# Optimization experiments

Hardware: AMD Instinct MI355X
Metric: run time of the kernel (lower is better)

Reference implementation:

```python
import jax, jax.numpy as jnp
import numpy as np

NEG_INF = -1e12
ALPHA = 0.01  # LeakyReLU slope


def setup_inputs() -> dict:
    key = jax.random.key(0)
    ks = jax.random.split(key, 12)
    K, N, DIN, H1, DOUT, FC1 = 64, 1024, 16, 4, 8, 54
    X = jax.random.normal(ks[0], (K, N, DIN), dtype=jnp.float32)
    adj = jax.random.randint(ks[1], (N, N), 0, 2, dtype=jnp.int32)
    # Xavier-uniform-ish init scale (gain 1.414)
    def xavier(k, shape):
        fan_in, fan_out = shape[0], shape[-1]
        lim = 1.414 * np.sqrt(6.0 / (fan_in + fan_out))
        return jax.random.uniform(k, shape, jnp.float32, -lim, lim)
    W1 = xavier(ks[2], (DIN, H1))
    a1 = xavier(ks[3], (2 * H1, 1))
    W2 = xavier(ks[4], (H1, DOUT))
    a2 = xavier(ks[5], (2 * DOUT, 1))
    fc1_w = xavier(ks[6], (N * DOUT, FC1))
    fc1_b = jnp.zeros((FC1,), jnp.float32)
    out_w = xavier(ks[7], (FC1, N))
    out_b = jnp.zeros((N,), jnp.float32)
    return {"X": X, "adj": adj, "W1": W1, "a1": a1, "W2": W2, "a2": a2,
            "fc1_w": fc1_w, "fc1_b": fc1_b, "out_w": out_w, "out_b": out_b}


def _gat_layer(h_in, adj, W, a):
    # h: [K, N, F]
    h = jnp.matmul(h_in, W)
    Fdim = W.shape[1]
    # concat(h_i, h_j) @ a  ==  (h_i . a[:F]) + (h_j . a[F:])
    f1 = jnp.matmul(h, a[:Fdim, 0])  # [K, N]
    f2 = jnp.matmul(h, a[Fdim:, 0])  # [K, N]
    e = jax.nn.leaky_relu(f1[:, :, None] + f2[:, None, :], ALPHA)  # [K, N, N]
    e = jnp.where(adj[None, :, :] > 0, e, NEG_INF)
    att = jax.nn.softmax(e, axis=2)
    return jnp.einsum('kij,kjf->kif', att, h)


def reference(X, adj, W1, a1, W2, a2, fc1_w, fc1_b, out_w, out_b):
    x = jax.nn.relu(_gat_layer(X, adj, W1, a1))
    x = jax.nn.relu(_gat_layer(x, adj, W2, a2))
    x = x.reshape(x.shape[0], -1)  # [K, N*dim_output]
    x = jax.nn.relu(jnp.matmul(x, fc1_w) + fc1_b)
    return jnp.matmul(x, out_w) + out_b  # [K, N] q-values
```

## Files before the change

### kernel.cpp

```cpp
#include <hip/hip_runtime.h>
#include <hip/hip_bf16.h>

constexpr int K    = 64;
constexpr int N    = 1024;
constexpr int DIN  = 16;
constexpr int H1   = 4;
constexpr int DOUT = 8;
constexpr int FC1  = 54;

#define ALPHA_F   (0.01f)
#define LOG2E_F   (1.4426950408889634f)

typedef unsigned int uint;
typedef short  bf16x8 __attribute__((ext_vector_type(8)));
typedef float  f32x4  __attribute__((ext_vector_type(4)));

__device__ inline float fast_exp2(float x) {
#if __has_builtin(__builtin_amdgcn_exp2f)
    return __builtin_amdgcn_exp2f(x);
#else
    return __expf(x * 0.6931471805599453f);
#endif
}

__device__ inline uint pk_bf16(float a, float b) {
    union { __hip_bfloat162 h; uint u; } v;
    v.h = __float22bfloat162_rn(make_float2(a, b));
    return v.u;
}


__global__ __launch_bounds__(512) void prep_kernel(
        const int* __restrict__ adj, unsigned long long* __restrict__ maskM,
        const float* __restrict__ fc1w, float* __restrict__ wt,
        const float* __restrict__ X, const float* __restrict__ W1,
        const float* __restrict__ a1,
        uint4* __restrict__ HB1, float* __restrict__ f11, float* __restrict__ f21) {
    int b = blockIdx.x;
    if (b < 2048) {
        int wave = threadIdx.x >> 6, lane = threadIdx.x & 63;
        int wid = b * 8 + wave;
        int jw  = wid >> 10;
        int i   = wid & 1023;
        int v = adj[i * N + (jw << 6) + lane];
        unsigned long long m = __ballot(v > 0);
        if (lane == 0) maskM[i * 16 + jw] = m;
    } else if (b < 2112) {
        __shared__ float tile[128 * FC1];
        const int m0 = (b - 2048) * 128;
        const float* src = fc1w + (size_t)m0 * FC1;
        for (int idx = threadIdx.x; idx < 128 * FC1; idx += 512)
            tile[idx] = src[idx];
        __syncthreads();
        for (int idx = threadIdx.x; idx < 128 * FC1; idx += 512) {
            int c = idx >> 7, mm = idx & 127;
            wt[(size_t)c * (N * DOUT) + m0 + mm] = tile[mm * FC1 + c];
        }
    } else {
        __shared__ float hrow[512 * 4];
        const int bb  = b - 2112;
        const int k   = bb >> 1;
        const int j0  = (bb & 1) * 512;
        const int tid = threadIdx.x;
        const int idx = k * N + j0 + tid;
        const float4* x4 = (const float4*)(X + (size_t)idx * DIN);
        float hv_[H1] = {0.f, 0.f, 0.f, 0.f};
        #pragma unroll
        for (int q = 0; q < 4; q++) {
            float4 xv = x4[q];
            #pragma unroll
            for (int f = 0; f < H1; f++) {
                hv_[f] += xv.x * W1[(q * 4 + 0) * H1 + f] + xv.y * W1[(q * 4 + 1) * H1 + f]
                        + xv.z * W1[(q * 4 + 2) * H1 + f] + xv.w * W1[(q * 4 + 3) * H1 + f];
            }
        }
        float s1 = 0.f, s2 = 0.f;
        #pragma unroll
        for (int f = 0; f < H1; f++) { s1 += hv_[f] * a1[f]; s2 += hv_[f] * a1[H1 + f]; }
        f11[idx] = s1 * LOG2E_F;
        f21[idx] = s2 * LOG2E_F;
        #pragma unroll
        for (int f = 0; f < H1; f++) hrow[tid * 4 + f] = hv_[f];
        __syncthreads();
        uint4* HBk = HB1 + (size_t)k * 2048 + (j0 >> 5) * 64;
        #pragma unroll
        for (int e = tid; e < 1024; e += 512) {
            int cl = e >> 6, l = e & 63, q = (l >> 4), n = l & 15;
            uint4 dw;
            if (n < H1) {
                const float* hp = hrow + (cl * 32 + q * 8) * 4 + n;
                dw.x = pk_bf16(hp[0],  hp[4]);
                dw.y = pk_bf16(hp[8],  hp[12]);
                dw.z = pk_bf16(hp[16], hp[20]);
                dw.w = pk_bf16(hp[24], hp[28]);
            } else if (n == H1) {
                dw = make_uint4(0x3f803f80u, 0x3f803f80u, 0x3f803f80u, 0x3f803f80u);
            } else {
                dw = make_uint4(0u, 0u, 0u, 0u);
            }
            HBk[cl * 64 + l] = dw;
        }
    }
}

template <int F, bool FUSE>
__global__ __launch_bounds__(512, 8) void gat_attn_mfma(
        const unsigned long long* __restrict__ maskM,
        const uint4* __restrict__ HBin,
        const float* __restrict__ f1,
        const float* __restrict__ f2,
        const float* __restrict__ W2,
        const float* __restrict__ a2,
        uint4* __restrict__ HBout,
        float* __restrict__ o_x,
        float* __restrict__ o_f1,
        float* __restrict__ o_f2) {
    __shared__ float F2s[1024];
    __shared__ float CMB[4][4][64];
    __shared__ float XPa[4][16][5];
    __shared__ float XPb[4][16][9];

    const int tid  = threadIdx.x;
    const int lane = tid & 63;
    const int wv   = tid >> 6;
    const int wt4  = wv & 3;
    const int jh   = wv >> 2;
    const int quad = lane >> 4;
    const int n16  = lane & 15;
    const int k    = blockIdx.x >> 4;

    if (tid < 256)
        ((float4*)F2s)[tid] = ((const float4*)(f2 + k * N))[tid];
    __syncthreads();

    const int itile = (blockIdx.x & 15) * 4 + wt4;
    const int ibase = itile * 16;
    const int irow  = ibase + n16;
    const float f1v = f1[k * N + irow];
    const uint4* mrow = (const uint4*)((const char*)maskM + (size_t)irow * 128) + jh * 4;
    const uint4* HBk  = HBin + (size_t)k * 2048 + jh * 1024;

    f32x4 acc = {0.f, 0.f, 0.f, 0.f};
    union { bf16x8 v; uint u[4]; } af;
    union { bf16x8 v; uint4 q; }  bfrag;

    #pragma unroll 2
    for (int g = 0; g < 4; g++) {
        const uint4 Mg = mrow[g];
        #pragma unroll
        for (int cc = 0; cc < 4; cc++) {
            const int cl = g * 4 + cc;
            const int c  = jh * 16 + cl;
            const uint mdw = (cc == 0) ? Mg.x : (cc == 1) ? Mg.y
                           : (cc == 2) ? Mg.z : Mg.w;
            const uint mb  = (mdw >> (quad * 8)) & 0xffu;
            bfrag.q = HBk[cl * 64 + lane];
            float4 fa = *(const float4*)(F2s + c * 32 + quad * 8);
            float4 fb = *(const float4*)(F2s + c * 32 + quad * 8 + 4);
            float f2e[8] = {fa.x, fa.y, fa.z, fa.w, fb.x, fb.y, fb.z, fb.w};
            float pv[8];
            #pragma unroll
            for (int jj = 0; jj < 8; jj++) {
                float x = f1v + f2e[jj];
                float e = fmaxf(x, ALPHA_F * x);
                float p = fast_exp2(e);
                pv[jj] = (mb & (1u << jj)) ? p : 0.f;
            }
            #pragma unroll
            for (int pr = 0; pr < 4; pr++)
                af.u[pr] = pk_bf16(pv[2 * pr], pv[2 * pr + 1]);
            acc = __builtin_amdgcn_mfma_f32_16x16x32_bf16(af.v, bfrag.v, acc, 0, 0, 0);
        }
    }

    if (jh == 1) {
        #pragma unroll
        for (int r = 0; r < 4; r++) CMB[wt4][r][lane] = acc[r];
    }
    __syncthreads();

    if (jh == 0) {
        #pragma unroll
        for (int r = 0; r < 4; r++) acc[r] += CMB[wt4][r][lane];
        #pragma unroll
        for (int r = 0; r < 4; r++) {
            float den = __shfl(acc[r], (lane & 48) + F);
            float inv = (den > 0.f) ? 1.f / den : 0.f;
            float xo  = fmaxf(acc[r] * inv, 0.f);
            int m = quad * 4 + r;
            if constexpr (FUSE) {
                if (n16 < F) XPa[wt4][m][n16] = xo;
            } else {
                if (n16 < F) o_x[((size_t)k * N + ibase + m) * F + n16] = xo;
            }
        }
    }

    if constexpr (FUSE) {
        __syncthreads();
        if (jh == 0 && lane < 16) {
            const int m = lane;
            float x0 = XPa[wt4][m][0], x1 = XPa[wt4][m][1];
            float x2v = XPa[wt4][m][2], x3 = XPa[wt4][m][3];
            float hv[DOUT];
            #pragma unroll
            for (int f = 0; f < DOUT; f++) {
                hv[f] = x0 * W2[f]      + x1 * W2[8 + f]
                      + x2v * W2[16 + f] + x3 * W2[24 + f];
            }
            float t1 = 0.f, t2 = 0.f;
            #pragma unroll
            for (int f = 0; f < DOUT; f++) { t1 += hv[f] * a2[f]; t2 += hv[f] * a2[DOUT + f]; }
            const int row = k * N + ibase + m;
            o_f1[row] = t1 * LOG2E_F;
            o_f2[row] = t2 * LOG2E_F;
            #pragma unroll
            for (int f = 0; f < DOUT; f++) XPb[wt4][m][f] = hv[f];
        }
        __syncthreads();
        if (jh == 0 && lane < 32) {
            const int c2    = ibase >> 5;
            const int qhalf = (ibase >> 4) & 1;
            const int ql    = lane >> 4;
            const int n     = lane & 15;
            const int q     = qhalf * 2 + ql;
            uint4 dw;
            if (n < DOUT) {
                dw.x = pk_bf16(XPb[wt4][ql * 8 + 0][n], XPb[wt4][ql * 8 + 1][n]);
                dw.y = pk_bf16(XPb[wt4][ql * 8 + 2][n], XPb[wt4][ql * 8 + 3][n]);
                dw.z = pk_bf16(XPb[wt4][ql * 8 + 4][n], XPb[wt4][ql * 8 + 5][n]);
                dw.w = pk_bf16(XPb[wt4][ql * 8 + 6][n], XPb[wt4][ql * 8 + 7][n]);
            } else if (n == DOUT) {
                dw = make_uint4(0x3f803f80u, 0x3f803f80u, 0x3f803f80u, 0x3f803f80u);
            } else {
                dw = make_uint4(0u, 0u, 0u, 0u);
            }
            HBout[(size_t)k * 2048 + c2 * 64 + q * 16 + n] = dw;
        }
    }
}

__global__ __launch_bounds__(256) void fc1_kernel(
        const float* __restrict__ x2, const float* __restrict__ wt,
        const float* __restrict__ b, float* __restrict__ y) {
    const int bid  = blockIdx.x;
    const int k    = bid / FC1;
    const int c    = bid - k * FC1;
    const int wave = threadIdx.x >> 6;
    const int lane = threadIdx.x & 63;
    const float4* x4 = (const float4*)(x2 + (size_t)k * N * DOUT) + wave * 512 + lane;
    const float4* w4 = (const float4*)(wt + (size_t)c * N * DOUT) + wave * 512 + lane;
    float s0 = 0.f, s1 = 0.f;
    #pragma unroll
    for (int q = 0; q < 8; q += 2) {
        float4 a0 = x4[q * 64],      w0 = w4[q * 64];
        float4 a1 = x4[q * 64 + 64], w1 = w4[q * 64 + 64];
        s0 += a0.x * w0.x + a0.y * w0.y + a0.z * w0.z + a0.w * w0.w;
        s1 += a1.x * w1.x + a1.y * w1.y + a1.z * w1.z + a1.w * w1.w;
    }
    float s = s0 + s1;
    #pragma unroll
    for (int off = 32; off > 0; off >>= 1) s += __shfl_xor(s, off);
    __shared__ float red[4];
    if (lane == 0) red[wave] = s;
    __syncthreads();
    if (threadIdx.x == 0)
        y[bid] = fmaxf(red[0] + red[1] + red[2] + red[3] + b[c], 0.f);
}

__global__ void fc2_kernel(const float* __restrict__ y,
                           const float* __restrict__ out_w,
                           const float* __restrict__ out_b,
                           float* __restrict__ out) {
    int n = blockIdx.x * blockDim.x + threadIdx.x;
    int k = blockIdx.y;
    const float* yk = y + (size_t)k * FC1;
    float s = out_b[n];
    #pragma unroll 6
    for (int c = 0; c < FC1; c++) s += yk[c] * out_w[(size_t)c * N + n];
    out[(size_t)k * N + n] = s;
}

extern "C" void kernel_launch(void* const* d_in, const int* in_sizes, int n_in,
                              void* d_out, int out_size, void* d_ws, size_t ws_size,
                              hipStream_t stream) {
    const float* X     = (const float*)d_in[0];
    const int*   adj   = (const int*)  d_in[1];
    const float* W1    = (const float*)d_in[2];
    const float* a1    = (const float*)d_in[3];
    const float* W2    = (const float*)d_in[4];
    const float* a2    = (const float*)d_in[5];
    const float* fc1w  = (const float*)d_in[6];
    const float* fc1b  = (const float*)d_in[7];
    const float* outw  = (const float*)d_in[8];
    const float* outb  = (const float*)d_in[9];
    float* out = (float*)d_out;

    float* ws  = (float*)d_ws;
    float* f11 = ws;
    float* f21 = f11 + 65536;
    float* f12 = f21 + 65536;
    float* f22 = f12 + 65536;
    float* x2  = f22 + 65536;
    float* y   = x2  + 524288;
    float* wt  = y   + 4096;
    unsigned long long* mM = (unsigned long long*)(wt + 442368);
    uint4* HB1 = (uint4*)(wt + 442368 + 32768);
    uint4* HB2 = HB1 + 131072;

    prep_kernel<<<dim3(2240), dim3(512), 0, stream>>>(
        adj, mM, fc1w, wt, X, W1, a1, HB1, f11, f21);

    gat_attn_mfma<4, true><<<dim3(K * 16), dim3(512), 0, stream>>>(
        mM, HB1, f11, f21, W2, a2, HB2, nullptr, f12, f22);

    gat_attn_mfma<8, false><<<dim3(K * 16), dim3(512), 0, stream>>>(
        mM, HB2, f12, f22, nullptr, nullptr, nullptr, x2, nullptr, nullptr);

    fc1_kernel<<<dim3(K * FC1), dim3(256), 0, stream>>>(x2, wt, fc1b, y);
    fc2_kernel<<<dim3(N / 256, K), dim3(256), 0, stream>>>(y, outw, outb, out);
}
```

Baseline: 134.8 us.

## Fuse all stages into one persistent cooperative kernel with grid syncs

```diff
diff --git a/kernel.cpp b/kernel.cpp
--- a/kernel.cpp
+++ b/kernel.cpp
@@ -1,5 +1,8 @@
 #include <hip/hip_runtime.h>
 #include <hip/hip_bf16.h>
+#include <hip/hip_cooperative_groups.h>
+
+namespace cg = cooperative_groups;
 
 constexpr int K    = 64;
 constexpr int N    = 1024;
@@ -29,96 +32,28 @@
     return v.u;
 }
 
-
-__global__ __launch_bounds__(512) void prep_kernel(
-        const int* __restrict__ adj, unsigned long long* __restrict__ maskM,
-        const float* __restrict__ fc1w, float* __restrict__ wt,
-        const float* __restrict__ X, const float* __restrict__ W1,
-        const float* __restrict__ a1,
-        uint4* __restrict__ HB1, float* __restrict__ f11, float* __restrict__ f21) {
-    int b = blockIdx.x;
-    if (b < 2048) {
-        int wave = threadIdx.x >> 6, lane = threadIdx.x & 63;
-        int wid = b * 8 + wave;
-        int jw  = wid >> 10;
-        int i   = wid & 1023;
-        int v = adj[i * N + (jw << 6) + lane];
-        unsigned long long m = __ballot(v > 0);
-        if (lane == 0) maskM[i * 16 + jw] = m;
-    } else if (b < 2112) {
-        __shared__ float tile[128 * FC1];
-        const int m0 = (b - 2048) * 128;
-        const float* src = fc1w + (size_t)m0 * FC1;
-        for (int idx = threadIdx.x; idx < 128 * FC1; idx += 512)
-            tile[idx] = src[idx];
-        __syncthreads();
-        for (int idx = threadIdx.x; idx < 128 * FC1; idx += 512) {
-            int c = idx >> 7, mm = idx & 127;
-            wt[(size_t)c * (N * DOUT) + m0 + mm] = tile[mm * FC1 + c];
-        }
-    } else {
-        __shared__ float hrow[512 * 4];
-        const int bb  = b - 2112;
-        const int k   = bb >> 1;
-        const int j0  = (bb & 1) * 512;
-        const int tid = threadIdx.x;
-        const int idx = k * N + j0 + tid;
-        const float4* x4 = (const float4*)(X + (size_t)idx * DIN);
-        float hv_[H1] = {0.f, 0.f, 0.f, 0.f};
-        #pragma unroll
-        for (int q = 0; q < 4; q++) {
-            float4 xv = x4[q];
-            #pragma unroll
-            for (int f = 0; f < H1; f++) {
-                hv_[f] += xv.x * W1[(q * 4 + 0) * H1 + f] + xv.y * W1[(q * 4 + 1) * H1 + f]
-                        + xv.z * W1[(q * 4 + 2) * H1 + f] + xv.w * W1[(q * 4 + 3) * H1 + f];
-            }
-        }
-        float s1 = 0.f, s2 = 0.f;
-        #pragma unroll
-        for (int f = 0; f < H1; f++) { s1 += hv_[f] * a1[f]; s2 += hv_[f] * a1[H1 + f]; }
-        f11[idx] = s1 * LOG2E_F;
-        f21[idx] = s2 * LOG2E_F;
-        #pragma unroll
-        for (int f = 0; f < H1; f++) hrow[tid * 4 + f] = hv_[f];
-        __syncthreads();
-        uint4* HBk = HB1 + (size_t)k * 2048 + (j0 >> 5) * 64;
-        #pragma unroll
-        for (int e = tid; e < 1024; e += 512) {
-            int cl = e >> 6, l = e & 63, q = (l >> 4), n = l & 15;
-            uint4 dw;
-            if (n < H1) {
-                const float* hp = hrow + (cl * 32 + q * 8) * 4 + n;
-                dw.x = pk_bf16(hp[0],  hp[4]);
-                dw.y = pk_bf16(hp[8],  hp[12]);
-                dw.z = pk_bf16(hp[16], hp[20]);
-                dw.w = pk_bf16(hp[24], hp[28]);
-            } else if (n == H1) {
-                dw = make_uint4(0x3f803f80u, 0x3f803f80u, 0x3f803f80u, 0x3f803f80u);
-            } else {
-                dw = make_uint4(0u, 0u, 0u, 0u);
-            }
-            HBk[cl * 64 + l] = dw;
-        }
-    }
-}
+struct Params {
+    const float* X; const int* adj; const float* W1; const float* a1;
+    const float* W2; const float* a2; const float* fc1w; const float* fc1b;
+    const float* outw; const float* outb; float* out;
+    float* f11; float* f21; float* f12; float* f22;
+    float* x2; float* y; float* wt;
+    unsigned long long* mM; uint4* HB1; uint4* HB2;
+};
 
 template <int F, bool FUSE>
-__global__ __launch_bounds__(512, 8) void gat_attn_mfma(
+__device__ __forceinline__ void attn_phase(
+        int t, char* smem,
         const unsigned long long* __restrict__ maskM,
         const uint4* __restrict__ HBin,
-        const float* __restrict__ f1,
-        const float* __restrict__ f2,
-        const float* __restrict__ W2,
-        const float* __restrict__ a2,
-        uint4* __restrict__ HBout,
-        float* __restrict__ o_x,
-        float* __restrict__ o_f1,
-        float* __restrict__ o_f2) {
-    __shared__ float F2s[1024];
-    __shared__ float CMB[4][4][64];
-    __shared__ float XPa[4][16][5];
-    __shared__ float XPb[4][16][9];
+        const float* __restrict__ f1, const float* __restrict__ f2,
+        const float* __restrict__ W2, const float* __restrict__ a2,
+        uint4* __restrict__ HBout, float* __restrict__ o_x,
+        float* __restrict__ o_f1, float* __restrict__ o_f2) {
+    float* F2s = (float*)smem;
+    float (*CMB)[4][64] = (float(*)[4][64])(smem + 4096);
+    float (*XPa)[16][5] = (float(*)[16][5])(smem + 8192);
+    float (*XPb)[16][9] = (float(*)[16][9])(smem + 9472);
 
     const int tid  = threadIdx.x;
     const int lane = tid & 63;
@@ -127,13 +62,13 @@
     const int jh   = wv >> 2;
     const int quad = lane >> 4;
     const int n16  = lane & 15;
-    const int k    = blockIdx.x >> 4;
+    const int k    = t >> 4;
 
     if (tid < 256)
         ((float4*)F2s)[tid] = ((const float4*)(f2 + k * N))[tid];
     __syncthreads();
 
-    const int itile = (blockIdx.x & 15) * 4 + wt4;
+    const int itile = (t & 15) * 4 + wt4;
     const int ibase = itile * 16;
     const int irow  = ibase + n16;
     const float f1v = f1[k * N + irow];
@@ -240,62 +175,128 @@
     }
 }
 
-__global__ __launch_bounds__(256) void fc1_kernel(
-        const float* __restrict__ x2, const float* __restrict__ wt,
-        const float* __restrict__ b, float* __restrict__ y) {
-    const int bid  = blockIdx.x;
-    const int k    = bid / FC1;
-    const int c    = bid - k * FC1;
-    const int wave = threadIdx.x >> 6;
-    const int lane = threadIdx.x & 63;
-    const float4* x4 = (const float4*)(x2 + (size_t)k * N * DOUT) + wave * 512 + lane;
-    const float4* w4 = (const float4*)(wt + (size_t)c * N * DOUT) + wave * 512 + lane;
-    float s0 = 0.f, s1 = 0.f;
-    #pragma unroll
-    for (int q = 0; q < 8; q += 2) {
-        float4 a0 = x4[q * 64],      w0 = w4[q * 64];
-        float4 a1 = x4[q * 64 + 64], w1 = w4[q * 64 + 64];
-        s0 += a0.x * w0.x + a0.y * w0.y + a0.z * w0.z + a0.w * w0.w;
-        s1 += a1.x * w1.x + a1.y * w1.y + a1.z * w1.z + a1.w * w1.w;
-    }
-    float s = s0 + s1;
-    #pragma unroll
-    for (int off = 32; off > 0; off >>= 1) s += __shfl_xor(s, off);
-    __shared__ float red[4];
-    if (lane == 0) red[wave] = s;
-    __syncthreads();
-    if (threadIdx.x == 0)
-        y[bid] = fmaxf(red[0] + red[1] + red[2] + red[3] + b[c], 0.f);
-}
-
-__global__ void fc2_kernel(const float* __restrict__ y,
-                           const float* __restrict__ out_w,
-                           const float* __restrict__ out_b,
-                           float* __restrict__ out) {
-    int n = blockIdx.x * blockDim.x + threadIdx.x;
-    int k = blockIdx.y;
-    const float* yk = y + (size_t)k * FC1;
-    float s = out_b[n];
-    #pragma unroll 6
-    for (int c = 0; c < FC1; c++) s += yk[c] * out_w[(size_t)c * N + n];
-    out[(size_t)k * N + n] = s;
+__global__ __launch_bounds__(512, 4) void mega(Params p) {
+    cg::grid_group grid = cg::this_grid();
+    __shared__ __align__(16) char smem[128 * FC1 * 4];
+    const int b   = blockIdx.x;
+    const int G   = gridDim.x;
+    const int tid = threadIdx.x;
+    const int wv  = tid >> 6, lane = tid & 63;
+
+    for (int t = b * 8 + wv; t < 16384; t += G * 8) {
+        int jw = t >> 10;
+        int i  = t & 1023;
+        int v = p.adj[i * N + (jw << 6) + lane];
+        unsigned long long m = __ballot(v > 0);
+        if (lane == 0) p.mM[i * 16 + jw] = m;
+    }
+    for (int bt = b; bt < 64; bt += G) {
+        float* tile = (float*)smem;
+        const int m0 = bt * 128;
+        const float* src = p.fc1w + (size_t)m0 * FC1;
+        __syncthreads();
+        for (int idx = tid; idx < 128 * FC1; idx += 512)
+            tile[idx] = src[idx];
+        __syncthreads();
+        for (int idx = tid; idx < 128 * FC1; idx += 512) {
+            int c = idx >> 7, mm = idx & 127;
+            p.wt[(size_t)c * (N * DOUT) + m0 + mm] = tile[mm * FC1 + c];
+        }
+        __syncthreads();
+    }
+    for (int bt = b; bt < 128; bt += G) {
+        float* hrow = (float*)smem;
+        const int k  = bt >> 1;
+        const int j0 = (bt & 1) * 512;
+        const int idx = k * N + j0 + tid;
+        const float4* x4 = (const float4*)(p.X + (size_t)idx * DIN);
+        float hv_[H1] = {0.f, 0.f, 0.f, 0.f};
+        #pragma unroll
+        for (int q = 0; q < 4; q++) {
+            float4 xv = x4[q];
+            #pragma unroll
+            for (int f = 0; f < H1; f++) {
+                hv_[f] += xv.x * p.W1[(q * 4 + 0) * H1 + f] + xv.y * p.W1[(q * 4 + 1) * H1 + f]
+                        + xv.z * p.W1[(q * 4 + 2) * H1 + f] + xv.w * p.W1[(q * 4 + 3) * H1 + f];
+            }
+        }
+        float s1 = 0.f, s2 = 0.f;
+        #pragma unroll
+        for (int f = 0; f < H1; f++) { s1 += hv_[f] * p.a1[f]; s2 += hv_[f] * p.a1[H1 + f]; }
+        p.f11[idx] = s1 * LOG2E_F;
+        p.f21[idx] = s2 * LOG2E_F;
+        __syncthreads();
+        #pragma unroll
+        for (int f = 0; f < H1; f++) hrow[tid * 4 + f] = hv_[f];
+        __syncthreads();
+        uint4* HBk = p.HB1 + (size_t)k * 2048 + (j0 >> 5) * 64;
+        #pragma unroll
+        for (int e = tid; e < 1024; e += 512) {
+            int cl = e >> 6, l = e & 63, q = (l >> 4), n = l & 15;
+            uint4 dw;
+            if (n < H1) {
+                const float* hp = hrow + (cl * 32 + q * 8) * 4 + n;
+                dw.x = pk_bf16(hp[0],  hp[4]);
+                dw.y = pk_bf16(hp[8],  hp[12]);
+                dw.z = pk_bf16(hp[16], hp[20]);
+                dw.w = pk_bf16(hp[24], hp[28]);
+            } else if (n == H1) {
+                dw = make_uint4(0x3f803f80u, 0x3f803f80u, 0x3f803f80u, 0x3f803f80u);
+            } else {
+                dw = make_uint4(0u, 0u, 0u, 0u);
+            }
+            HBk[cl * 64 + l] = dw;
+        }
+        __syncthreads();
+    }
+    grid.sync();
+
+    for (int t = b; t < 1024; t += G) {
+        attn_phase<4, true>(t, smem, p.mM, p.HB1, p.f11, p.f21, p.W2, p.a2,
+                            p.HB2, nullptr, p.f12, p.f22);
+        __syncthreads();
+    }
+    grid.sync();
+
+    for (int t = b; t < 1024; t += G) {
+        attn_phase<8, false>(t, smem, p.mM, p.HB2, p.f12, p.f22, nullptr,
+                             nullptr, nullptr, p.x2, nullptr, nullptr);
+        __syncthreads();
+    }
+    grid.sync();
+
+    for (int gw = b * 8 + wv; gw < K * FC1; gw += G * 8) {
+        const int k = gw / FC1, c = gw - k * FC1;
+        const float4* x4 = (const float4*)(p.x2 + (size_t)k * N * DOUT);
+        const float4* w4 = (const float4*)(p.wt + (size_t)c * N * DOUT);
+        float s0 = 0.f, s1 = 0.f;
+        #pragma unroll 8
+        for (int q = 0; q < 32; q += 2) {
+            float4 a0 = x4[q * 64 + lane],       w0 = w4[q * 64 + lane];
+            float4 a1 = x4[(q + 1) * 64 + lane], w1 = w4[(q + 1) * 64 + lane];
+            s0 += a0.x * w0.x + a0.y * w0.y + a0.z * w0.z + a0.w * w0.w;
+            s1 += a1.x * w1.x + a1.y * w1.y + a1.z * w1.z + a1.w * w1.w;
+        }
+        float s = s0 + s1;
+        #pragma unroll
+        for (int off = 32; off > 0; off >>= 1) s += __shfl_xor(s, off);
+        if (lane == 0) p.y[gw] = fmaxf(s + p.fc1b[c], 0.f);
+    }
+    grid.sync();
+
+    for (int idx = b * 512 + tid; idx < K * N; idx += G * 512) {
+        const int k = idx >> 10, n = idx & 1023;
+        const float* yk = p.y + (size_t)k * FC1;
+        float s = p.outb[n];
+        #pragma unroll 6
+        for (int c = 0; c < FC1; c++) s += yk[c] * p.outw[(size_t)c * N + n];
+        p.out[idx] = s;
+    }
 }
 
 extern "C" void kernel_launch(void* const* d_in, const int* in_sizes, int n_in,
                               void* d_out, int out_size, void* d_ws, size_t ws_size,
                               hipStream_t stream) {
-    const float* X     = (const float*)d_in[0];
-    const int*   adj   = (const int*)  d_in[1];
-    const float* W1    = (const float*)d_in[2];
-    const float* a1    = (const float*)d_in[3];
-    const float* W2    = (const float*)d_in[4];
-    const float* a2    = (const float*)d_in[5];
-    const float* fc1w  = (const float*)d_in[6];
-    const float* fc1b  = (const float*)d_in[7];
-    const float* outw  = (const float*)d_in[8];
-    const float* outb  = (const float*)d_in[9];
-    float* out = (float*)d_out;
-
     float* ws  = (float*)d_ws;
     float* f11 = ws;
     float* f21 = f11 + 65536;
@@ -308,15 +309,33 @@
     uint4* HB1 = (uint4*)(wt + 442368 + 32768);
     uint4* HB2 = HB1 + 131072;
 
-    prep_kernel<<<dim3(2240), dim3(512), 0, stream>>>(
-        adj, mM, fc1w, wt, X, W1, a1, HB1, f11, f21);
-
-    gat_attn_mfma<4, true><<<dim3(K * 16), dim3(512), 0, stream>>>(
-        mM, HB1, f11, f21, W2, a2, HB2, nullptr, f12, f22);
-
-    gat_attn_mfma<8, false><<<dim3(K * 16), dim3(512), 0, stream>>>(
-        mM, HB2, f12, f22, nullptr, nullptr, nullptr, x2, nullptr, nullptr);
-
-    fc1_kernel<<<dim3(K * FC1), dim3(256), 0, stream>>>(x2, wt, fc1b, y);
-    fc2_kernel<<<dim3(N / 256, K), dim3(256), 0, stream>>>(y, outw, outb, out);
-}
+    Params p;
+    p.X    = (const float*)d_in[0];
+    p.adj  = (const int*)  d_in[1];
+    p.W1   = (const float*)d_in[2];
+    p.a1   = (const float*)d_in[3];
+    p.W2   = (const float*)d_in[4];
+    p.a2   = (const float*)d_in[5];
+    p.fc1w = (const float*)d_in[6];
+    p.fc1b = (const float*)d_in[7];
+    p.outw = (const float*)d_in[8];
+    p.outb = (const float*)d_in[9];
+    p.out  = (float*)d_out;
+    p.f11 = f11; p.f21 = f21; p.f12 = f12; p.f22 = f22;
+    p.x2 = x2; p.y = y; p.wt = wt;
+    p.mM = mM; p.HB1 = HB1; p.HB2 = HB2;
+
+    int dev = 0;
+    hipGetDevice(&dev);
+    int nCU = 256;
+    hipDeviceGetAttribute(&nCU, hipDeviceAttributeMultiprocessorCount, dev);
+    int maxB = 0;
+    hipOccupancyMaxActiveBlocksPerMultiprocessor(&maxB, mega, 512, 0);
+    if (maxB < 1) maxB = 1;
+    int G = maxB * nCU;
+    if (G > 1024) G = 1024;
+
+    void* args[] = { &p };
+    hipLaunchCooperativeKernel((const void*)mega, dim3(G), dim3(512),
+                               args, 0, stream);
+}
```

Result: slower. 287.7 us (+113.4%).

## Expand adjacency mask to bf16 AND-masks in MFMA fragment layout

Applied to the files above, without the earlier changes.

```diff
diff --git a/kernel.cpp b/kernel.cpp
--- a/kernel.cpp
+++ b/kernel.cpp
@@ -31,23 +31,29 @@
 
 
 __global__ __launch_bounds__(512) void prep_kernel(
-        const int* __restrict__ adj, unsigned long long* __restrict__ maskM,
+        const int* __restrict__ adj, uint4* __restrict__ EM,
         const float* __restrict__ fc1w, float* __restrict__ wt,
         const float* __restrict__ X, const float* __restrict__ W1,
         const float* __restrict__ a1,
         uint4* __restrict__ HB1, float* __restrict__ f11, float* __restrict__ f21) {
     int b = blockIdx.x;
-    if (b < 2048) {
-        int wave = threadIdx.x >> 6, lane = threadIdx.x & 63;
-        int wid = b * 8 + wave;
-        int jw  = wid >> 10;
-        int i   = wid & 1023;
-        int v = adj[i * N + (jw << 6) + lane];
-        unsigned long long m = __ballot(v > 0);
-        if (lane == 0) maskM[i * 16 + jw] = m;
-    } else if (b < 2112) {
+    if (b < 256) {
+        const int e     = b * 512 + threadIdx.x;
+        const int lane  = e & 63;
+        const int itile = (e >> 6) & 63;
+        const int c     = e >> 12;
+        const int i     = itile * 16 + (lane & 15);
+        const int j0    = c * 32 + (lane >> 4) * 8;
+        const int* ap   = adj + (size_t)i * N + j0;
+        uint4 m;
+        m.x = (ap[0] > 0 ? 0x0000FFFFu : 0u) | (ap[1] > 0 ? 0xFFFF0000u : 0u);
+        m.y = (ap[2] > 0 ? 0x0000FFFFu : 0u) | (ap[3] > 0 ? 0xFFFF0000u : 0u);
+        m.z = (ap[4] > 0 ? 0x0000FFFFu : 0u) | (ap[5] > 0 ? 0xFFFF0000u : 0u);
+        m.w = (ap[6] > 0 ? 0x0000FFFFu : 0u) | (ap[7] > 0 ? 0xFFFF0000u : 0u);
+        EM[e] = m;
+    } else if (b < 320) {
         __shared__ float tile[128 * FC1];
-        const int m0 = (b - 2048) * 128;
+        const int m0 = (b - 256) * 128;
         const float* src = fc1w + (size_t)m0 * FC1;
         for (int idx = threadIdx.x; idx < 128 * FC1; idx += 512)
             tile[idx] = src[idx];
@@ -58,7 +64,7 @@
         }
     } else {
         __shared__ float hrow[512 * 4];
-        const int bb  = b - 2112;
+        const int bb  = b - 320;
         const int k   = bb >> 1;
         const int j0  = (bb & 1) * 512;
         const int tid = threadIdx.x;
@@ -104,8 +110,8 @@
 }
 
 template <int F, bool FUSE>
-__global__ __launch_bounds__(512, 8) void gat_attn_mfma(
-        const unsigned long long* __restrict__ maskM,
+__global__ __launch_bounds__(512, 4) void gat_attn_mfma(
+        const uint4* __restrict__ EM,
         const uint4* __restrict__ HBin,
         const float* __restrict__ f1,
         const float* __restrict__ f2,
@@ -115,7 +121,6 @@
         float* __restrict__ o_x,
         float* __restrict__ o_f1,
         float* __restrict__ o_f2) {
-    __shared__ float F2s[1024];
     __shared__ float CMB[4][4][64];
     __shared__ float XPa[4][16][5];
     __shared__ float XPb[4][16][9];
@@ -129,48 +134,38 @@
     const int n16  = lane & 15;
     const int k    = blockIdx.x >> 4;
 
-    if (tid < 256)
-        ((float4*)F2s)[tid] = ((const float4*)(f2 + k * N))[tid];
-    __syncthreads();
-
     const int itile = (blockIdx.x & 15) * 4 + wt4;
     const int ibase = itile * 16;
     const int irow  = ibase + n16;
     const float f1v = f1[k * N + irow];
-    const uint4* mrow = (const uint4*)((const char*)maskM + (size_t)irow * 128) + jh * 4;
+    const float* f2k  = f2 + k * N + quad * 8;
     const uint4* HBk  = HBin + (size_t)k * 2048 + jh * 1024;
+    const uint4* EMk  = EM + ((size_t)(jh * 16) * 64 + itile) * 64 + lane;
 
     f32x4 acc = {0.f, 0.f, 0.f, 0.f};
     union { bf16x8 v; uint u[4]; } af;
     union { bf16x8 v; uint4 q; }  bfrag;
 
-    #pragma unroll 2
-    for (int g = 0; g < 4; g++) {
-        const uint4 Mg = mrow[g];
-        #pragma unroll
-        for (int cc = 0; cc < 4; cc++) {
-            const int cl = g * 4 + cc;
-            const int c  = jh * 16 + cl;
-            const uint mdw = (cc == 0) ? Mg.x : (cc == 1) ? Mg.y
-                           : (cc == 2) ? Mg.z : Mg.w;
-            const uint mb  = (mdw >> (quad * 8)) & 0xffu;
-            bfrag.q = HBk[cl * 64 + lane];
-            float4 fa = *(const float4*)(F2s + c * 32 + quad * 8);
-            float4 fb = *(const float4*)(F2s + c * 32 + quad * 8 + 4);
-            float f2e[8] = {fa.x, fa.y, fa.z, fa.w, fb.x, fb.y, fb.z, fb.w};
-            float pv[8];
-            #pragma unroll
-            for (int jj = 0; jj < 8; jj++) {
-                float x = f1v + f2e[jj];
-                float e = fmaxf(x, ALPHA_F * x);
-                float p = fast_exp2(e);
-                pv[jj] = (mb & (1u << jj)) ? p : 0.f;
-            }
-            #pragma unroll
-            for (int pr = 0; pr < 4; pr++)
-                af.u[pr] = pk_bf16(pv[2 * pr], pv[2 * pr + 1]);
-            acc = __builtin_amdgcn_mfma_f32_16x16x32_bf16(af.v, bfrag.v, acc, 0, 0, 0);
-        }
+    #pragma unroll 4
+    for (int cl = 0; cl < 16; cl++) {
+        const int c = jh * 16 + cl;
+        bfrag.q = HBk[cl * 64 + lane];
+        const uint4 em = EMk[(size_t)cl * 4096];
+        float4 fa = *(const float4*)(f2k + c * 32);
+        float4 fb = *(const float4*)(f2k + c * 32 + 4);
+        float f2e[8] = {fa.x, fa.y, fa.z, fa.w, fb.x, fb.y, fb.z, fb.w};
+        float pv[8];
+        #pragma unroll
+        for (int jj = 0; jj < 8; jj++) {
+            float x = f1v + f2e[jj];
+            float e = fmaxf(x, ALPHA_F * x);
+            pv[jj] = fast_exp2(e);
+        }
+        af.u[0] = pk_bf16(pv[0], pv[1]) & em.x;
+        af.u[1] = pk_bf16(pv[2], pv[3]) & em.y;
+        af.u[2] = pk_bf16(pv[4], pv[5]) & em.z;
+        af.u[3] = pk_bf16(pv[6], pv[7]) & em.w;
+        acc = __builtin_amdgcn_mfma_f32_16x16x32_bf16(af.v, bfrag.v, acc, 0, 0, 0);
     }
 
     if (jh == 1) {
@@ -304,18 +299,18 @@
     float* x2  = f22 + 65536;
     float* y   = x2  + 524288;
     float* wt  = y   + 4096;
-    unsigned long long* mM = (unsigned long long*)(wt + 442368);
-    uint4* HB1 = (uint4*)(wt + 442368 + 32768);
+    uint4* HB1 = (uint4*)(wt + 442368);
     uint4* HB2 = HB1 + 131072;
-
-    prep_kernel<<<dim3(2240), dim3(512), 0, stream>>>(
-        adj, mM, fc1w, wt, X, W1, a1, HB1, f11, f21);
+    uint4* EMt = HB2 + 131072;
+
+    prep_kernel<<<dim3(448), dim3(512), 0, stream>>>(
+        adj, EMt, fc1w, wt, X, W1, a1, HB1, f11, f21);
 
     gat_attn_mfma<4, true><<<dim3(K * 16), dim3(512), 0, stream>>>(
-        mM, HB1, f11, f21, W2, a2, HB2, nullptr, f12, f22);
+        EMt, HB1, f11, f21, W2, a2, HB2, nullptr, f12, f22);
 
     gat_attn_mfma<8, false><<<dim3(K * 16), dim3(512), 0, stream>>>(
-        mM, HB2, f12, f22, nullptr, nullptr, nullptr, x2, nullptr, nullptr);
+        EMt, HB2, f12, f22, nullptr, nullptr, nullptr, x2, nullptr, nullptr);
 
     fc1_kernel<<<dim3(K * FC1), dim3(256), 0, stream>>>(x2, wt, fc1b, y);
     fc2_kernel<<<dim3(N / 256, K), dim3(256), 0, stream>>>(y, outw, outb, out);
```

Result: no change. 135.4 us (+0.4%).
